# Optimization experiments

Measured on AMD Instinct MI355X. Metric: run time of the kernel, lower is better.

## Reference

```python
import jax, jax.numpy as jnp
import numpy as np

N, E, R = 100000, 600000, 2      # nodes, edges per relation, relations
IN, H, DH = 128, 8, 16           # input dim, heads, per-head hidden
D = H * DH                       # 128 = hidden_dim * n_heads
RIN, RH = 64, 16                 # relation input / hidden dims
SLOPE = 0.2                      # leaky relu negative slope


def _leaky(v):
    return jnp.where(v >= 0, v, SLOPE * v)


def setup_inputs() -> dict:
    key = jax.random.key(0)
    ks = jax.random.split(key, 18)
    nrm = lambda k, shape, s: jax.random.normal(k, shape, jnp.float32) * s
    sc = 1.0 / np.sqrt(D).astype(np.float32)
    return {
        'x': nrm(ks[0], (N, IN), 1.0),
        'src': jax.random.randint(ks[1], (R, E), 0, N, jnp.int32),
        'dst': jax.random.randint(ks[2], (R, E), 0, N, jnp.int32),
        'rel_emb': nrm(ks[3], (R, RIN), 1.0),
        'Wp': nrm(ks[4], (IN, D), sc), 'bp': jnp.zeros((D,), jnp.float32),
        'Wn': nrm(ks[5], (D, D), sc), 'bn': jnp.zeros((D,), jnp.float32),
        'Wsrc': nrm(ks[6], (R, D, D), sc), 'bsrc': jnp.zeros((R, D), jnp.float32),
        'Wrel': nrm(ks[7], (R, RIN, H * 2 * DH), 1.0 / np.sqrt(RIN).astype(np.float32)),
        'resW': nrm(ks[8], (IN, D), sc), 'resb': jnp.zeros((D,), jnp.float32),
        'res_alpha': nrm(ks[9], (1,), 1.0),
        'crossW': nrm(ks[10], (R, H, DH), 1.0 / np.sqrt(DH).astype(np.float32)),
        'Wprop': nrm(ks[11], (R, RIN, H * RH), 1.0 / np.sqrt(RIN).astype(np.float32)),
        'bprop': jnp.zeros((R, H * RH), jnp.float32),
    }


def reference(x, src, dst, rel_emb, Wp, bp, Wn, bn, Wsrc, bsrc, Wrel,
              resW, resb, res_alpha, crossW, Wprop, bprop):
    # projection_layer (R_HGT) then node_transformation_layers (layer input transform)
    xp = x @ Wp + bp                                  # [N, D]
    h = (xp @ Wn + bn).reshape(N, H, DH)              # [N, H, DH] dst-side features
    res = (xp @ resW + resb).reshape(N, H, DH)        # res_fc(input_dst)

    def per_rel(sr, dr, e_emb, Ws, bs, Wr):
        # relation_src_node_transformation + relation-conditioned attention
        s = (h.reshape(N, D) @ Ws + bs).reshape(N, H, DH)   # src messages
        a = (e_emb @ Wr).reshape(H, 2, DH)                  # relation attn vectors
        sc_src = (s * a[:, 0]).sum(-1)                      # [N, H]
        sc_dst = (h * a[:, 1]).sum(-1)                      # [N, H]
        e_sc = _leaky(sc_src[sr] + sc_dst[dr])              # [E, H]
        # edge softmax over incoming edges of each dst node
        m = jax.lax.stop_gradient(jax.ops.segment_max(e_sc, dr, num_segments=N))
        ex = jnp.exp(e_sc - m[dr])
        den = jax.ops.segment_sum(ex, dr, num_segments=N)
        alpha = ex / den[dr]                                # [E, H]
        msg = alpha[:, :, None] * s[sr]                     # [E, H, DH]
        return jax.ops.segment_sum(msg, dr, num_segments=N)  # [N, H, DH]

    out = jax.vmap(per_rel)(src, dst, rel_emb, Wsrc, bsrc, Wrel)  # [R, N, H, DH]

    # sigmoid-gated residual (shared per dst ntype)
    g = jax.nn.sigmoid(res_alpha)[0]
    out = out * g + res[None] * (1.0 - g)

    # RelationCrossing: attention across the R relation-specific dst features
    def cross(cw):
        attn = jax.nn.softmax(_leaky((out * cw[None, None]).sum(-1)), axis=0)  # [R,N,H]
        return (attn[..., None] * out).sum(0)                                  # [N,H,DH]

    fused = jax.vmap(cross)(crossW).reshape(R, N, D)      # [R, N, D]

    # relation_propagation_layer
    rel_out = jnp.einsum('ri,rio->ro', rel_emb, Wprop) + bprop  # [R, H*RH]
    return fused, rel_out
```

## Files before the change

kernel.cpp:

```cpp
#include <hip/hip_runtime.h>
#include <math.h>

#define NN 100000
#define EE 600000
#define RR 2
#define DD 128
#define HH 8
#define DHH 16
#define RN (RR * NN)
#define NT 26
#define MTOT 6250
#define NB3 ((MTOT + 3) / 4)
#define CHUNK 4096
#define NCH ((EE + CHUNK - 1) / CHUNK)
#define BINW 512
#define NBIN ((NN + BINW - 1) / BINW)
#define BCAPD 4096

typedef unsigned short ushort_t;
typedef short bf16x8 __attribute__((ext_vector_type(8)));
typedef float f32x4 __attribute__((ext_vector_type(4)));
typedef unsigned short u16x4 __attribute__((ext_vector_type(4)));

__device__ __forceinline__ float lrelu(float v) { return v >= 0.f ? v : 0.2f * v; }

__device__ __forceinline__ ushort_t f2bf(float f) {
    unsigned int u = __float_as_uint(f);
    u = (u + 0x7FFFu + ((u >> 16) & 1u)) >> 16;
    return (ushort_t)u;
}
__device__ __forceinline__ float bf2f(ushort_t u) {
    return __uint_as_float(((unsigned int)u) << 16);
}

__global__ __launch_bounds__(128) void k_compose1(
    const float* __restrict__ Wp, const float* __restrict__ bp,
    const float* __restrict__ Wn, const float* __restrict__ bn,
    const float* __restrict__ resW, const float* __restrict__ resb,
    const float* __restrict__ rel_emb, const float* __restrict__ Wrel,
    const float* __restrict__ Wprop, const float* __restrict__ bprop,
    const int* __restrict__ dst, int* __restrict__ binct,
    float* __restrict__ Wpn, float* __restrict__ bpn,
    float* __restrict__ Wres_c, float* __restrict__ bres_c,
    float* __restrict__ avec, float* __restrict__ rel_out) {
    const int tid = threadIdx.x;
    if (blockIdx.x >= DD) {
        __shared__ int bins[NBIN];
        const int b = blockIdx.x - DD;
        const int rel = b / NCH, blk = b - rel * NCH;
        for (int i = tid; i < NBIN; i += 128) bins[i] = 0;
        __syncthreads();
        for (int i = tid; i < CHUNK; i += 128) {
            int e = blk * CHUNK + i;
            if (e < EE)
                atomicAdd(&bins[__builtin_nontemporal_load(dst + rel * EE + e) >> 9], 1);
        }
        __syncthreads();
        for (int i = tid; i < NBIN; i += 128)
            binct[((rel * NCH) + blk) * NBIN + i] = bins[i];
        return;
    }
    __shared__ float row[DD];
    const int rrow = blockIdx.x;
    row[tid] = Wp[rrow * DD + tid];
    __syncthreads();
    float acc1 = 0.f, acc2 = 0.f;
    for (int k = 0; k < DD; ++k) {
        float wv = row[k];
        acc1 = fmaf(wv, Wn[k * DD + tid], acc1);
        acc2 = fmaf(wv, resW[k * DD + tid], acc2);
    }
    Wpn[rrow * DD + tid] = acc1;
    Wres_c[rrow * DD + tid] = acc2;
    if (rrow == 0) {
        float b1 = 0.f, b2 = 0.f;
        for (int k = 0; k < DD; ++k) {
            b1 = fmaf(bp[k], Wn[k * DD + tid], b1);
            b2 = fmaf(bp[k], resW[k * DD + tid], b2);
        }
        bpn[tid] = b1 + bn[tid];
        bres_c[tid] = b2 + resb[tid];
    }
    if (rrow < 4) {
        int idx = rrow * DD + tid;
        int r = idx >> 8, o = idx & 255;
        float acc = 0.f;
        for (int i = 0; i < 64; ++i)
            acc += rel_emb[r * 64 + i] * Wrel[(r * 64 + i) * 256 + o];
        avec[idx] = acc;
    } else if (rrow < 6) {
        int o = (rrow - 4) * DD + tid;
        int r = o >> 7, oo = o & 127;
        float acc = bprop[o];
        for (int i = 0; i < 64; ++i)
            acc += rel_emb[r * 64 + i] * Wprop[(r * 64 + i) * 128 + oo];
        rel_out[o] = acc;
    }
}

__global__ __launch_bounds__(128) void k_compose2(
    const float* __restrict__ Wpn, const float* __restrict__ bpn,
    const float* __restrict__ Wsrc, const float* __restrict__ bsrc,
    const float* __restrict__ avec,
    const int* __restrict__ binct, int* __restrict__ runoff,
    int* __restrict__ binstart, int* __restrict__ row_ptr,
    float* __restrict__ Ws_c, float* __restrict__ bs_c,
    float* __restrict__ VdstT, float* __restrict__ cdst) {
    const int tid = threadIdx.x;
    if (blockIdx.y == DD) {
        if (blockIdx.x != 0) return;
        __shared__ int part[128];
        int s[4];
        #pragma unroll
        for (int q = 0; q < 4; ++q) {
            int pb = tid * 4 + q;
            int run = 0;
            if (pb < RR * NBIN) {
                int rel = pb / NBIN, bin = pb - rel * NBIN;
                for (int blk = 0; blk < NCH; ++blk) {
                    int idx = ((rel * NCH) + blk) * NBIN + bin;
                    int v = binct[idx];
                    runoff[idx] = run;
                    run += v;
                }
            }
            s[q] = run;
        }
        part[tid] = s[0] + s[1] + s[2] + s[3];
        __syncthreads();
        for (int off = 1; off < 128; off <<= 1) {
            int v = (tid >= off) ? part[tid - off] : 0;
            __syncthreads();
            part[tid] += v;
            __syncthreads();
        }
        int excl = (tid == 0) ? 0 : part[tid - 1];
        binstart[4 * tid]     = excl;
        binstart[4 * tid + 1] = excl + s[0];
        binstart[4 * tid + 2] = excl + s[0] + s[1];
        binstart[4 * tid + 3] = excl + s[0] + s[1] + s[2];
        if (tid == 0) row_ptr[RN] = RR * EE;
        return;
    }
    __shared__ float row[DD];
    const int rel = blockIdx.x, rrow = blockIdx.y;
    row[tid] = Wpn[rrow * DD + tid];
    __syncthreads();
    const float* W = Wsrc + (size_t)rel * DD * DD;
    float acc = 0.f;
    for (int k = 0; k < DD; ++k) acc = fmaf(row[k], W[k * DD + tid], acc);
    Ws_c[(size_t)rel * DD * DD + rrow * DD + tid] = acc;
    if (tid < HH) {
        float v = 0.f;
        for (int d = 0; d < 16; ++d)
            v += row[tid * 16 + d] * avec[rel * 256 + tid * 32 + 16 + d];
        VdstT[(rel * HH + tid) * DD + rrow] = v;
    }
    if (rrow == 0) {
        float b = 0.f;
        for (int k = 0; k < DD; ++k) b = fmaf(bpn[k], W[k * DD + tid], b);
        bs_c[rel * DD + tid] = b + bsrc[rel * DD + tid];
        if (rel == 0 && tid < 16) {
            int r2 = tid >> 3, h2 = tid & 7;
            float c2 = 0.f;
            for (int d = 0; d < 16; ++d)
                c2 += bpn[h2 * 16 + d] * avec[r2 * 256 + h2 * 32 + 16 + d];
            cdst[tid] = c2;
        }
    }
}

__global__ __launch_bounds__(256) void k_pack(
    const float* __restrict__ Ws_c, const float* __restrict__ Wres_c,
    const float* __restrict__ VdstT, const float* __restrict__ avec,
    const float* __restrict__ bs_c,
    const int* __restrict__ src, const int* __restrict__ dst,
    const int* __restrict__ runoff, const int* __restrict__ binstart,
    int* __restrict__ ebuf,
    short* __restrict__ Wpk, float* __restrict__ csrc) {
    const int tid = threadIdx.x;
    if (blockIdx.x >= NT) {
        __shared__ int ofs[NBIN];
        __shared__ int bins[NBIN];
        const int b = blockIdx.x - NT;
        const int rel = b / NCH, blk = b - rel * NCH;
        if (tid < NBIN) {
            ofs[tid] = binstart[rel * NBIN + tid] +
                       runoff[((rel * NCH) + blk) * NBIN + tid];
            bins[tid] = 0;
        }
        __syncthreads();
        for (int i = tid; i < CHUNK; i += 256) {
            int e = blk * CHUNK + i;
            if (e < EE) {
                int d = __builtin_nontemporal_load(dst + rel * EE + e);
                int bb = d >> 9;
                int loc = atomicAdd(&bins[bb], 1);
                ebuf[ofs[bb] + loc] =
                    ((d & 511) << 17) | __builtin_nontemporal_load(src + rel * EE + e);
            }
        }
        return;
    }
    const int t = blockIdx.x;
    const int kt = tid >> 6;
    const int l = tid & 63;
    const int c16 = l & 15;
    bf16x8 v;
    #pragma unroll
    for (int j = 0; j < 8; ++j) {
        int k = kt * 32 + (l >> 4) * 8 + j;
        float f;
        if (t < 24) {
            int m = t >> 3;
            int col = (t & 7) * 16 + c16;
            const float* W = (m == 0) ? Ws_c : (m == 1) ? Ws_c + DD * DD : Wres_c;
            f = W[k * DD + col];
        } else if (t == 24) {
            f = VdstT[c16 * DD + k];
        } else {
            int rel = c16 >> 3, h = c16 & 7;
            f = 0.f;
            for (int d = 0; d < 16; ++d)
                f += Ws_c[(size_t)rel * DD * DD + k * DD + h * 16 + d]
                     * avec[rel * 256 + h * 32 + d];
        }
        v[j] = (short)f2bf(f);
    }
    *(bf16x8*)(Wpk + ((size_t)(t * 4 + kt) * 64 + l) * 8) = v;
    if (t == 25 && tid < 16) {
        int rel = tid >> 3, h = tid & 7;
        float c = 0.f;
        for (int d = 0; d < 16; ++d)
            c += bs_c[rel * DD + h * 16 + d] * avec[rel * 256 + h * 32 + d];
        csrc[tid] = c;
    }
}

__global__ __launch_bounds__(256) void k_node3(
    const float* __restrict__ x, const short* __restrict__ Wpk,
    const float* __restrict__ bs_c, const float* __restrict__ bres_c,
    const float* __restrict__ cdst, const float* __restrict__ csrc,
    const int* __restrict__ ebuf, const int* __restrict__ binstart,
    int* __restrict__ row_ptr, int* __restrict__ esrc,
    ushort_t* __restrict__ s_out, ushort_t* __restrict__ res_out,
    float* __restrict__ sc_src, float* __restrict__ sc_dst) {
    const int tid = threadIdx.x;
    if (blockIdx.x >= NB3) {
        __shared__ int keys[BCAPD];
        __shared__ int cnt[BINW];
        __shared__ int scn[BINW];
        __shared__ int part[256];
        const int b = blockIdx.x - NB3;
        const int rel = b / NBIN, bin = b - rel * NBIN;
        const int p0 = binstart[rel * NBIN + bin];
        const int p1 = binstart[rel * NBIN + bin + 1];
        const int cntE = p1 - p0;
        const bool inlds = (cntE <= BCAPD);
        const int n0 = bin * BINW;
        const int nw = min(BINW, NN - n0);

        cnt[2 * tid] = 0; cnt[2 * tid + 1] = 0;
        __syncthreads();
        for (int i = tid; i < cntE; i += 256) {
            int k = __builtin_nontemporal_load(ebuf + p0 + i);
            if (inlds) keys[i] = k;
            atomicAdd(&cnt[k >> 17], 1);
        }
        __syncthreads();
        int a = cnt[2 * tid], c = cnt[2 * tid + 1];
        part[tid] = a + c;
        __syncthreads();
        for (int off = 1; off < 256; off <<= 1) {
            int v = (tid >= off) ? part[tid - off] : 0;
            __syncthreads();
            part[tid] += v;
            __syncthreads();
        }
        int excl = (tid == 0) ? 0 : part[tid - 1];
        scn[2 * tid] = excl;
        scn[2 * tid + 1] = excl + a;
        cnt[2 * tid] = 0; cnt[2 * tid + 1] = 0;
        __syncthreads();
        for (int n = tid; n < nw; n += 256)
            row_ptr[rel * NN + n0 + n] = p0 + scn[n];
        for (int i = tid; i < cntE; i += 256) {
            int k = inlds ? keys[i] : ebuf[p0 + i];
            int low = k >> 17;
            int slot = atomicAdd(&cnt[low], 1);
            esrc[p0 + scn[low] + slot] = k & 0x1FFFF;
        }
        return;
    }
    const int l = tid & 63;
    const int w = tid >> 6;
    const int m16 = l & 15, g4 = l >> 4;
    const int mt = blockIdx.x * 4 + w;
    const bool live = (mt < MTOT);
    const int nb = (live ? mt : MTOT - 1) * 16;

    bf16x8 af[4];
    const float* xrow = x + (size_t)(nb + m16) * DD + g4 * 8;
    #pragma unroll
    for (int kt = 0; kt < 4; ++kt) {
        float4 v0 = *(const float4*)(xrow + kt * 32);
        float4 v1 = *(const float4*)(xrow + kt * 32 + 4);
        af[kt][0] = (short)f2bf(v0.x); af[kt][1] = (short)f2bf(v0.y);
        af[kt][2] = (short)f2bf(v0.z); af[kt][3] = (short)f2bf(v0.w);
        af[kt][4] = (short)f2bf(v1.x); af[kt][5] = (short)f2bf(v1.y);
        af[kt][6] = (short)f2bf(v1.z); af[kt][7] = (short)f2bf(v1.w);
    }

    for (int t = 0; t < NT; ++t) {
        f32x4 acc = {0.f, 0.f, 0.f, 0.f};
        #pragma unroll
        for (int kt = 0; kt < 4; ++kt) {
            bf16x8 b = *(const bf16x8*)(Wpk + ((size_t)(t * 4 + kt) * 64 + l) * 8);
            acc = __builtin_amdgcn_mfma_f32_16x16x32_bf16(af[kt], b, acc, 0, 0, 0);
        }
        if (!live) continue;
        if (t < 16) {
            const int rel = t >> 3, head = t & 7;
            const float bb = bs_c[rel * DD + head * 16 + m16];
            #pragma unroll
            for (int r = 0; r < 4; ++r) {
                const int node = nb + g4 * 4 + r;
                s_out[((size_t)rel * NN + node) * DD + head * 16 + m16] =
                    f2bf(acc[r] + bb);
            }
        } else if (t < 24) {
            const int col = (t - 16) * 16 + m16;
            const float bb = bres_c[col];
            #pragma unroll
            for (int r = 0; r < 4; ++r) {
                const int node = nb + g4 * 4 + r;
                res_out[(size_t)node * DD + col] = f2bf(acc[r] + bb);
            }
        } else if (t == 24) {
            const int rel = m16 >> 3, head = m16 & 7;
            const float bb = cdst[m16];
            #pragma unroll
            for (int r = 0; r < 4; ++r) {
                const int node = nb + g4 * 4 + r;
                sc_dst[((size_t)rel * NN + node) * HH + head] = acc[r] + bb;
            }
        } else {
            const int rel = m16 >> 3, head = m16 & 7;
            const float bb = csrc[m16];
            #pragma unroll
            for (int r = 0; r < 4; ++r) {
                const int node = nb + g4 * 4 + r;
                sc_src[((size_t)rel * NN + node) * HH + head] = acc[r] + bb;
            }
        }
    }
}

__global__ __launch_bounds__(256) void k_gather_cross(
    const int* __restrict__ esrc, const int* __restrict__ row_ptr,
    const float* __restrict__ sc_src, const float* __restrict__ sc_dst,
    const ushort_t* __restrict__ s, const ushort_t* __restrict__ res_buf,
    const float* __restrict__ res_alpha, const float* __restrict__ crossW,
    float* __restrict__ out) {
    int n = blockIdx.x * 4 + (threadIdx.x >> 6);
    if (n >= NN) return;
    const int lane = threadIdx.x & 63;
    const int g = lane >> 5;
    const int j = lane & 31;
    const int h = j >> 2;

    const int seg = g * NN + n;
    const int p0 = row_ptr[seg], p1 = row_ptr[seg + 1];
    const float sd = sc_dst[(size_t)seg * HH + h];

    float den0 = 0.f, den1 = 0.f;
    float4 acc0 = {0.f, 0.f, 0.f, 0.f}, acc1 = {0.f, 0.f, 0.f, 0.f};
    int p = p0;
    for (; p + 1 < p1; p += 2) {
        int sr0 = esrc[p], sr1 = esrc[p + 1];
        ushort4 s40 = *(const ushort4*)(s + (size_t)(g * NN + sr0) * DD + j * 4);
        ushort4 s41 = *(const ushort4*)(s + (size_t)(g * NN + sr1) * DD + j * 4);
        float v0 = lrelu(sc_src[(size_t)(g * NN + sr0) * HH + h] + sd);
        float v1 = lrelu(sc_src[(size_t)(g * NN + sr1) * HH + h] + sd);
        float e0 = __expf(v0);
        float e1 = __expf(v1);
        den0 += e0; den1 += e1;
        acc0.x = fmaf(e0, bf2f(s40.x), acc0.x); acc1.x = fmaf(e1, bf2f(s41.x), acc1.x);
        acc0.y = fmaf(e0, bf2f(s40.y), acc0.y); acc1.y = fmaf(e1, bf2f(s41.y), acc1.y);
        acc0.z = fmaf(e0, bf2f(s40.z), acc0.z); acc1.z = fmaf(e1, bf2f(s41.z), acc1.z);
        acc0.w = fmaf(e0, bf2f(s40.w), acc0.w); acc1.w = fmaf(e1, bf2f(s41.w), acc1.w);
    }
    if (p < p1) {
        int sr0 = esrc[p];
        ushort4 s40 = *(const ushort4*)(s + (size_t)(g * NN + sr0) * DD + j * 4);
        float v0 = lrelu(sc_src[(size_t)(g * NN + sr0) * HH + h] + sd);
        float e0 = __expf(v0);
        den0 += e0;
        acc0.x = fmaf(e0, bf2f(s40.x), acc0.x);
        acc0.y = fmaf(e0, bf2f(s40.y), acc0.y);
        acc0.z = fmaf(e0, bf2f(s40.z), acc0.z);
        acc0.w = fmaf(e0, bf2f(s40.w), acc0.w);
    }
    float den = den0 + den1;
    float4 acc = {acc0.x + acc1.x, acc0.y + acc1.y, acc0.z + acc1.z, acc0.w + acc1.w};
    float inv = (p1 > p0) ? 1.f / den : 0.f;

    float gate = 1.f / (1.f + __expf(-res_alpha[0]));
    u16x4 r4u = __builtin_nontemporal_load(
        (const u16x4*)(res_buf + (size_t)n * DD + j * 4));
    float4 og;
    og.x = fmaf(acc.x * inv, gate, bf2f(r4u[0]) * (1.f - gate));
    og.y = fmaf(acc.y * inv, gate, bf2f(r4u[1]) * (1.f - gate));
    og.z = fmaf(acc.z * inv, gate, bf2f(r4u[2]) * (1.f - gate));
    og.w = fmaf(acc.w * inv, gate, bf2f(r4u[3]) * (1.f - gate));

    float4 oo;
    oo.x = __shfl_xor(og.x, 32);
    oo.y = __shfl_xor(og.y, 32);
    oo.z = __shfl_xor(og.z, 32);
    oo.w = __shfl_xor(og.w, 32);

    float4 cw = *(const float4*)(crossW + g * DD + j * 4);
    float ds_ = og.x * cw.x + og.y * cw.y + og.z * cw.z + og.w * cw.w;
    float do_ = oo.x * cw.x + oo.y * cw.y + oo.z * cw.z + oo.w * cw.w;
    ds_ += __shfl_xor(ds_, 1); ds_ += __shfl_xor(ds_, 2);
    do_ += __shfl_xor(do_, 1); do_ += __shfl_xor(do_, 2);
    float l0 = lrelu(ds_), l1 = lrelu(do_);
    float mm = fmaxf(l0, l1);
    float e0 = __expf(l0 - mm), e1 = __expf(l1 - mm);
    float winv = 1.f / (e0 + e1);
    float w0 = e0 * winv, w1 = e1 * winv;

    f32x4 o;
    o[0] = w0 * og.x + w1 * oo.x;
    o[1] = w0 * og.y + w1 * oo.y;
    o[2] = w0 * og.z + w1 * oo.z;
    o[3] = w0 * og.w + w1 * oo.w;
    __builtin_nontemporal_store(o, (f32x4*)(out + (size_t)(g * NN + n) * DD + j * 4));
}

extern "C" void kernel_launch(void* const* d_in, const int* in_sizes, int n_in,
                              void* d_out, int out_size, void* d_ws, size_t ws_size,
                              hipStream_t stream) {
    const float* x        = (const float*)d_in[0];
    const int*   src      = (const int*)d_in[1];
    const int*   dst      = (const int*)d_in[2];
    const float* rel_emb  = (const float*)d_in[3];
    const float* Wp       = (const float*)d_in[4];
    const float* bp       = (const float*)d_in[5];
    const float* Wn       = (const float*)d_in[6];
    const float* bn       = (const float*)d_in[7];
    const float* Wsrc     = (const float*)d_in[8];
    const float* bsrc     = (const float*)d_in[9];
    const float* Wrel     = (const float*)d_in[10];
    const float* resW     = (const float*)d_in[11];
    const float* resb     = (const float*)d_in[12];
    const float* res_alpha= (const float*)d_in[13];
    const float* crossW   = (const float*)d_in[14];
    const float* Wprop    = (const float*)d_in[15];
    const float* bprop    = (const float*)d_in[16];

    float* out = (float*)d_out;

    ushort_t* s_bf   = (ushort_t*)d_ws;
    ushort_t* res_bf = s_bf + (size_t)RR * NN * DD;
    float* fbase   = (float*)(res_bf + (size_t)NN * DD);
    float* sc_src  = fbase;
    float* sc_dst  = sc_src  + (size_t)RR * NN * HH;
    float* avec    = sc_dst  + (size_t)RR * NN * HH;
    float* Wpn     = avec    + 512;
    float* Wres_c  = Wpn     + DD * DD;
    float* Ws_c    = Wres_c  + DD * DD;
    float* VdstT   = Ws_c    + (size_t)RR * DD * DD;
    float* bpn     = VdstT   + 16 * DD;
    float* bres_c  = bpn     + DD;
    float* bs_c    = bres_c  + DD;
    float* cdst    = bs_c    + RR * DD;
    float* csrc    = cdst    + 16;
    short* Wpk     = (short*)(csrc + 16);
    int*   row_ptr = (int*)(Wpk + (size_t)NT * 4 * 64 * 8);
    int*   binct   = row_ptr + RN + 1;
    int*   runoff  = binct + RR * NCH * NBIN;
    int*   binstart= runoff + RR * NCH * NBIN;
    int*   ebuf    = binstart + 520;
    int*   esrc    = ebuf + RR * EE;

    k_compose1<<<DD + RR * NCH, 128, 0, stream>>>(
        Wp, bp, Wn, bn, resW, resb, rel_emb, Wrel, Wprop, bprop,
        dst, binct, Wpn, bpn, Wres_c, bres_c,
        avec, out + (size_t)RR * NN * DD);
    k_compose2<<<dim3(RR, DD + 1), 128, 0, stream>>>(
        Wpn, bpn, Wsrc, bsrc, avec, binct, runoff, binstart, row_ptr,
        Ws_c, bs_c, VdstT, cdst);
    k_pack<<<NT + RR * NCH, 256, 0, stream>>>(
        Ws_c, Wres_c, VdstT, avec, bs_c, src, dst, runoff, binstart, ebuf,
        Wpk, csrc);
    k_node3<<<NB3 + RR * NBIN, 256, 0, stream>>>(
        x, Wpk, bs_c, bres_c, cdst, csrc, ebuf, binstart, row_ptr, esrc,
        s_bf, res_bf, sc_src, sc_dst);
    k_gather_cross<<<(NN + 3) / 4, 256, 0, stream>>>(esrc, row_ptr, sc_src, sc_dst,
                                                     s_bf, res_bf, res_alpha, crossW,
                                                     out);
}
```

Baseline: 201.7 us.

## Parallelize bin-offset scan across blocks and add nontemporal loads/stores

Before, one block serially scanned the per-chunk bin counts. Now each histogram block atomically adds its counts into per-bin totals. k_compose2 launches one block per (relation, bin) to compute the chunk-wise exclusive prefix of run offsets in parallel, plus one block that scans the bin totals into binstart. The aim is to remove a long single-block serial loop from the critical path, at the cost of an extra memset, global atomics and more blocks. Separately, x loads, s/res stores and esrc loads become nontemporal to reduce cache pollution.

```diff
diff --git a/kernel.cpp b/kernel.cpp
--- a/kernel.cpp
+++ b/kernel.cpp
@@ -39,7 +39,7 @@
     const float* __restrict__ resW, const float* __restrict__ resb,
     const float* __restrict__ rel_emb, const float* __restrict__ Wrel,
     const float* __restrict__ Wprop, const float* __restrict__ bprop,
-    const int* __restrict__ dst, int* __restrict__ binct,
+    const int* __restrict__ dst, int* __restrict__ binct, int* __restrict__ bintot,
     float* __restrict__ Wpn, float* __restrict__ bpn,
     float* __restrict__ Wres_c, float* __restrict__ bres_c,
     float* __restrict__ avec, float* __restrict__ rel_out) {
@@ -56,8 +56,11 @@
                 atomicAdd(&bins[__builtin_nontemporal_load(dst + rel * EE + e) >> 9], 1);
         }
         __syncthreads();
-        for (int i = tid; i < NBIN; i += 128)
-            binct[((rel * NCH) + blk) * NBIN + i] = bins[i];
+        for (int i = tid; i < NBIN; i += 128) {
+            int v = bins[i];
+            binct[((rel * NCH) + blk) * NBIN + i] = v;
+            if (v) atomicAdd(&bintot[rel * NBIN + i], v);
+        }
         return;
     }
     __shared__ float row[DD];
@@ -102,44 +105,53 @@
     const float* __restrict__ Wpn, const float* __restrict__ bpn,
     const float* __restrict__ Wsrc, const float* __restrict__ bsrc,
     const float* __restrict__ avec,
-    const int* __restrict__ binct, int* __restrict__ runoff,
-    int* __restrict__ binstart, int* __restrict__ row_ptr,
+    const int* __restrict__ binct, const int* __restrict__ bintot,
+    int* __restrict__ runoff, int* __restrict__ binstart,
+    int* __restrict__ row_ptr,
     float* __restrict__ Ws_c, float* __restrict__ bs_c,
     float* __restrict__ VdstT, float* __restrict__ cdst) {
     const int tid = threadIdx.x;
-    if (blockIdx.y == DD) {
-        if (blockIdx.x != 0) return;
+    if (blockIdx.y >= DD) {
         __shared__ int part[128];
-        int s[4];
-        #pragma unroll
-        for (int q = 0; q < 4; ++q) {
-            int pb = tid * 4 + q;
-            int run = 0;
-            if (pb < RR * NBIN) {
-                int rel = pb / NBIN, bin = pb - rel * NBIN;
-                for (int blk = 0; blk < NCH; ++blk) {
-                    int idx = ((rel * NCH) + blk) * NBIN + bin;
-                    int v = binct[idx];
-                    runoff[idx] = run;
-                    run += v;
-                }
-            }
-            s[q] = run;
-        }
-        part[tid] = s[0] + s[1] + s[2] + s[3];
-        __syncthreads();
-        for (int off = 1; off < 128; off <<= 1) {
-            int v = (tid >= off) ? part[tid - off] : 0;
+        const int sidx = (blockIdx.y - DD) * RR + blockIdx.x;
+        if (sidx < RR * NBIN) {
+            const int rel = sidx / NBIN, bin = sidx - rel * NBIN;
+            int v0 = 0, v1 = 0;
+            const int c0 = 2 * tid, c1 = 2 * tid + 1;
+            if (c0 < NCH) v0 = binct[((rel * NCH) + c0) * NBIN + bin];
+            if (c1 < NCH) v1 = binct[((rel * NCH) + c1) * NBIN + bin];
+            part[tid] = v0 + v1;
             __syncthreads();
-            part[tid] += v;
+            for (int off = 1; off < 128; off <<= 1) {
+                int v = (tid >= off) ? part[tid - off] : 0;
+                __syncthreads();
+                part[tid] += v;
+                __syncthreads();
+            }
+            int excl = (tid == 0) ? 0 : part[tid - 1];
+            if (c0 < NCH) runoff[((rel * NCH) + c0) * NBIN + bin] = excl;
+            if (c1 < NCH) runoff[((rel * NCH) + c1) * NBIN + bin] = excl + v0;
+        } else if (sidx == RR * NBIN + (512 - RR * NBIN)) {
+        }
+        if (sidx == 512) {
+            int s[4];
+            #pragma unroll
+            for (int q = 0; q < 4; ++q) s[q] = bintot[4 * tid + q];
+            part[tid] = s[0] + s[1] + s[2] + s[3];
             __syncthreads();
-        }
-        int excl = (tid == 0) ? 0 : part[tid - 1];
-        binstart[4 * tid]     = excl;
-        binstart[4 * tid + 1] = excl + s[0];
-        binstart[4 * tid + 2] = excl + s[0] + s[1];
-        binstart[4 * tid + 3] = excl + s[0] + s[1] + s[2];
-        if (tid == 0) row_ptr[RN] = RR * EE;
+            for (int off = 1; off < 128; off <<= 1) {
+                int v = (tid >= off) ? part[tid - off] : 0;
+                __syncthreads();
+                part[tid] += v;
+                __syncthreads();
+            }
+            int excl = (tid == 0) ? 0 : part[tid - 1];
+            binstart[4 * tid]     = excl;
+            binstart[4 * tid + 1] = excl + s[0];
+            binstart[4 * tid + 2] = excl + s[0] + s[1];
+            binstart[4 * tid + 3] = excl + s[0] + s[1] + s[2];
+            if (tid == 0) row_ptr[RN] = RR * EE;
+        }
         return;
     }
     __shared__ float row[DD];
@@ -303,12 +315,12 @@
     const float* xrow = x + (size_t)(nb + m16) * DD + g4 * 8;
     #pragma unroll
     for (int kt = 0; kt < 4; ++kt) {
-        float4 v0 = *(const float4*)(xrow + kt * 32);
-        float4 v1 = *(const float4*)(xrow + kt * 32 + 4);
-        af[kt][0] = (short)f2bf(v0.x); af[kt][1] = (short)f2bf(v0.y);
-        af[kt][2] = (short)f2bf(v0.z); af[kt][3] = (short)f2bf(v0.w);
-        af[kt][4] = (short)f2bf(v1.x); af[kt][5] = (short)f2bf(v1.y);
-        af[kt][6] = (short)f2bf(v1.z); af[kt][7] = (short)f2bf(v1.w);
+        f32x4 v0 = __builtin_nontemporal_load((const f32x4*)(xrow + kt * 32));
+        f32x4 v1 = __builtin_nontemporal_load((const f32x4*)(xrow + kt * 32 + 4));
+        af[kt][0] = (short)f2bf(v0[0]); af[kt][1] = (short)f2bf(v0[1]);
+        af[kt][2] = (short)f2bf(v0[2]); af[kt][3] = (short)f2bf(v0[3]);
+        af[kt][4] = (short)f2bf(v1[0]); af[kt][5] = (short)f2bf(v1[1]);
+        af[kt][6] = (short)f2bf(v1[2]); af[kt][7] = (short)f2bf(v1[3]);
     }
 
     for (int t = 0; t < NT; ++t) {
@@ -325,8 +337,9 @@
             #pragma unroll
             for (int r = 0; r < 4; ++r) {
                 const int node = nb + g4 * 4 + r;
-                s_out[((size_t)rel * NN + node) * DD + head * 16 + m16] =
-                    f2bf(acc[r] + bb);
+                __builtin_nontemporal_store(
+                    f2bf(acc[r] + bb),
+                    s_out + ((size_t)rel * NN + node) * DD + head * 16 + m16);
             }
         } else if (t < 24) {
             const int col = (t - 16) * 16 + m16;
@@ -334,7 +347,8 @@
             #pragma unroll
             for (int r = 0; r < 4; ++r) {
                 const int node = nb + g4 * 4 + r;
-                res_out[(size_t)node * DD + col] = f2bf(acc[r] + bb);
+                __builtin_nontemporal_store(
+                    f2bf(acc[r] + bb), res_out + (size_t)node * DD + col);
             }
         } else if (t == 24) {
             const int rel = m16 >> 3, head = m16 & 7;
@@ -377,7 +391,8 @@
     float4 acc0 = {0.f, 0.f, 0.f, 0.f}, acc1 = {0.f, 0.f, 0.f, 0.f};
     int p = p0;
     for (; p + 1 < p1; p += 2) {
-        int sr0 = esrc[p], sr1 = esrc[p + 1];
+        int sr0 = __builtin_nontemporal_load(esrc + p);
+        int sr1 = __builtin_nontemporal_load(esrc + p + 1);
         ushort4 s40 = *(const ushort4*)(s + (size_t)(g * NN + sr0) * DD + j * 4);
         ushort4 s41 = *(const ushort4*)(s + (size_t)(g * NN + sr1) * DD + j * 4);
         float v0 = lrelu(sc_src[(size_t)(g * NN + sr0) * HH + h] + sd);
@@ -391,7 +406,7 @@
         acc0.w = fmaf(e0, bf2f(s40.w), acc0.w); acc1.w = fmaf(e1, bf2f(s41.w), acc1.w);
     }
     if (p < p1) {
-        int sr0 = esrc[p];
+        int sr0 = __builtin_nontemporal_load(esrc + p);
         ushort4 s40 = *(const ushort4*)(s + (size_t)(g * NN + sr0) * DD + j * 4);
         float v0 = lrelu(sc_src[(size_t)(g * NN + sr0) * HH + h] + sd);
         float e0 = __expf(v0);
@@ -482,15 +497,17 @@
     int*   binct   = row_ptr + RN + 1;
     int*   runoff  = binct + RR * NCH * NBIN;
     int*   binstart= runoff + RR * NCH * NBIN;
-    int*   ebuf    = binstart + 520;
+    int*   bintot  = binstart + 520;
+    int*   ebuf    = bintot + 512;
     int*   esrc    = ebuf + RR * EE;
 
+    hipMemsetAsync(bintot, 0, 512 * sizeof(int), stream);
     k_compose1<<<DD + RR * NCH, 128, 0, stream>>>(
         Wp, bp, Wn, bn, resW, resb, rel_emb, Wrel, Wprop, bprop,
-        dst, binct, Wpn, bpn, Wres_c, bres_c,
+        dst, binct, bintot, Wpn, bpn, Wres_c, bres_c,
         avec, out + (size_t)RR * NN * DD);
-    k_compose2<<<dim3(RR, DD + 1), 128, 0, stream>>>(
-        Wpn, bpn, Wsrc, bsrc, avec, binct, runoff, binstart, row_ptr,
+    k_compose2<<<dim3(RR, DD + 257), 128, 0, stream>>>(
+        Wpn, bpn, Wsrc, bsrc, avec, binct, bintot, runoff, binstart, row_ptr,
         Ws_c, bs_c, VdstT, cdst);
     k_pack<<<NT + RR * NCH, 256, 0, stream>>>(
         Ws_c, Wres_c, VdstT, avec, bs_c, src, dst, runoff, binstart, ebuf,
```

After: 260.2 us. 1.29x slower.
